# Optimization experiments

Measured on AMD Instinct MI355X. Metric: run time of the kernel, lower is better.

Reference implementation:

```python
import jax, jax.numpy as jnp
import numpy as np

C = 256; NH = 8; HD = C // NH; NL = 4; NP = 4; DFF = 1024
B = 8; NQ = 900
SHAPES = ((100, 100), (50, 50), (25, 25), (13, 13))
LEN = sum(h * w for h, w in SHAPES)


def setup_inputs() -> dict:
    key = jax.random.key(0)
    ks = jax.random.split(key, 16)
    s = 0.02
    d = {}
    d['tgt'] = jax.random.normal(ks[0], (B, NQ, C), jnp.float32)
    d['query_pos'] = jax.random.normal(ks[1], (B, NQ, C), jnp.float32)
    d['reference_points'] = jax.random.uniform(ks[2], (B, NQ, NL, 2), jnp.float32)
    d['src'] = jax.random.normal(ks[3], (B, LEN, C), jnp.float32)
    d['spatial_shapes'] = np.array(SHAPES, dtype=np.int32)
    # self-attn (nn.MultiheadAttention) params, stored [in,out]
    d['sa_in_w'] = jax.random.normal(ks[4], (C, 3 * C), jnp.float32) * s
    d['sa_in_b'] = jnp.zeros((3 * C,), jnp.float32)
    d['sa_out_w'] = jax.random.normal(ks[5], (C, C), jnp.float32) * s
    d['sa_out_b'] = jnp.zeros((C,), jnp.float32)
    d['ln2_g'] = jnp.ones((C,), jnp.float32); d['ln2_b'] = jnp.zeros((C,), jnp.float32)
    # MSDeformAttn params
    d['off_w'] = jax.random.normal(ks[6], (C, NH * NL * NP * 2), jnp.float32) * s
    d['off_b'] = jax.random.normal(ks[7], (NH * NL * NP * 2,), jnp.float32) * 0.5
    d['attw_w'] = jax.random.normal(ks[8], (C, NH * NL * NP), jnp.float32) * s
    d['attw_b'] = jnp.zeros((NH * NL * NP,), jnp.float32)
    d['val_w'] = jax.random.normal(ks[9], (C, C), jnp.float32) * s
    d['val_b'] = jnp.zeros((C,), jnp.float32)
    d['proj_w'] = jax.random.normal(ks[10], (C, C), jnp.float32) * s
    d['proj_b'] = jnp.zeros((C,), jnp.float32)
    d['ln1_g'] = jnp.ones((C,), jnp.float32); d['ln1_b'] = jnp.zeros((C,), jnp.float32)
    # FFN
    d['lin1_w'] = jax.random.normal(ks[11], (C, DFF), jnp.float32) * s
    d['lin1_b'] = jnp.zeros((DFF,), jnp.float32)
    d['lin2_w'] = jax.random.normal(ks[12], (DFF, C), jnp.float32) * s
    d['lin2_b'] = jnp.zeros((C,), jnp.float32)
    d['ln3_g'] = jnp.ones((C,), jnp.float32); d['ln3_b'] = jnp.zeros((C,), jnp.float32)
    return d


def _ln(x, g, b):
    m = jnp.mean(x, -1, keepdims=True)
    v = jnp.mean((x - m) ** 2, -1, keepdims=True)
    return (x - m) * jax.lax.rsqrt(v + 1e-5) * g + b


def _bilinear(v, loc, H, W):
    # v: [B,NH,H*W,HD]; loc: [B,NQ,NH,NP,2] normalized to [0,1]
    # matches F.grid_sample(align_corners=False, padding_mode='zeros')
    b = v.shape[0]; nq = loc.shape[1]
    x = loc[..., 0] * W - 0.5
    y = loc[..., 1] * H - 0.5
    x0 = jnp.floor(x); y0 = jnp.floor(y)
    dx = x - x0; dy = y - y0
    x0i = x0.astype(jnp.int32); y0i = y0.astype(jnp.int32)

    def gat(ix, iy):
        valid = ((ix >= 0) & (ix < W) & (iy >= 0) & (iy < H)).astype(v.dtype)
        idx = jnp.clip(iy, 0, H - 1) * W + jnp.clip(ix, 0, W - 1)  # [B,NQ,NH,NP]
        idx_t = jnp.transpose(idx, (0, 2, 1, 3)).reshape(b, NH, nq * NP)
        g = jnp.take_along_axis(v, idx_t[..., None], axis=2).reshape(b, NH, nq, NP, HD)
        return g * jnp.transpose(valid, (0, 2, 1, 3))[..., None]

    wt = lambda a: jnp.transpose(a, (0, 2, 1, 3))[..., None]
    return (gat(x0i, y0i) * wt((1 - dx) * (1 - dy))
            + gat(x0i + 1, y0i) * wt(dx * (1 - dy))
            + gat(x0i, y0i + 1) * wt((1 - dx) * dy)
            + gat(x0i + 1, y0i + 1) * wt(dx * dy))


def _msda(q, ref, src, shapes, val_w, val_b, off_w, off_b, attw_w, attw_b, proj_w, proj_b):
    b, nq, _ = q.shape
    value = jnp.transpose((src @ val_w + val_b).reshape(b, -1, NH, HD), (0, 2, 1, 3))  # [B,NH,Len,HD]
    off = (q @ off_w + off_b).reshape(b, nq, NH, NL, NP, 2)
    aw = jax.nn.softmax((q @ attw_w + attw_b).reshape(b, nq, NH, NL * NP), -1)
    aw = aw.reshape(b, nq, NH, NL, NP)
    acc = jnp.zeros((b, NH, nq, HD), q.dtype)
    start = 0
    for l, (H_, W_) in enumerate(shapes):
        norm = jnp.array([W_, H_], q.dtype)
        loc = ref[:, :, None, l, None, :] + off[:, :, :, l] / norm  # [B,NQ,NH,NP,2]
        smp = _bilinear(value[:, :, start:start + H_ * W_], loc, H_, W_)  # [B,NH,NQ,NP,HD]
        acc = acc + jnp.sum(smp * jnp.transpose(aw[:, :, :, l], (0, 2, 1, 3))[..., None], axis=3)
        start += H_ * W_
    out = jnp.transpose(acc, (0, 2, 1, 3)).reshape(b, nq, C)
    return out @ proj_w + proj_b


def _self_attn(x, pos, in_w, in_b, out_w, out_b):
    b, nq, _ = x.shape
    qk = x + pos
    q = (qk @ in_w[:, :C] + in_b[:C]).reshape(b, nq, NH, HD)
    k = (qk @ in_w[:, C:2 * C] + in_b[C:2 * C]).reshape(b, nq, NH, HD)
    v = (x @ in_w[:, 2 * C:] + in_b[2 * C:]).reshape(b, nq, NH, HD)
    att = jax.nn.softmax(jnp.einsum('bqhd,bkhd->bhqk', q, k) * (1.0 / float(np.sqrt(HD))), -1)
    o = jnp.einsum('bhqk,bkhd->bqhd', att, v).reshape(b, nq, C)
    return o @ out_w + out_b


def _forward(tgt, query_pos, reference_points, src, shapes,
             sa_in_w, sa_in_b, sa_out_w, sa_out_b, ln2_g, ln2_b,
             off_w, off_b, attw_w, attw_b, val_w, val_b, proj_w, proj_b, ln1_g, ln1_b,
             lin1_w, lin1_b, lin2_w, lin2_b, ln3_g, ln3_b):
    t2 = _self_attn(tgt, query_pos, sa_in_w, sa_in_b, sa_out_w, sa_out_b)
    t = _ln(tgt + t2, ln2_g, ln2_b)
    t2 = _msda(t + query_pos, reference_points, src, shapes,
               val_w, val_b, off_w, off_b, attw_w, attw_b, proj_w, proj_b)
    t = _ln(t + t2, ln1_g, ln1_b)
    h = jax.nn.relu(t @ lin1_w + lin1_b) @ lin2_w + lin2_b
    return _ln(t + h, ln3_g, ln3_b)


def reference(tgt, query_pos, reference_points, src, spatial_shapes,
              sa_in_w, sa_in_b, sa_out_w, sa_out_b, ln2_g, ln2_b,
              off_w, off_b, attw_w, attw_b, val_w, val_b, proj_w, proj_b, ln1_g, ln1_b,
              lin1_w, lin1_b, lin2_w, lin2_b, ln3_g, ln3_b):
    shapes = [(int(h), int(w)) for h, w in np.asarray(spatial_shapes)]
    return _forward(tgt, query_pos, reference_points, src, shapes,
                    sa_in_w, sa_in_b, sa_out_w, sa_out_b, ln2_g, ln2_b,
                    off_w, off_b, attw_w, attw_b, val_w, val_b, proj_w, proj_b, ln1_g, ln1_b,
                    lin1_w, lin1_b, lin2_w, lin2_b, ln3_g, ln3_b)
```

## Files before the change

### kernel.cpp

```cpp
#include <hip/hip_runtime.h>
#include <hip/hip_bf16.h>
#include <type_traits>

#define C_DIM 256
#define NHEAD 8
#define HDIM 32
#define NLVL 4
#define NPT 4
#define DFF_DIM 1024
#define BB 8
#define NQ_DIM 900
#define LEN_DIM 13294
#define ROWS (BB * NQ_DIM)
#define VROWS (BB * LEN_DIM)
#define VT_LD 928

typedef __attribute__((ext_vector_type(8))) short short8v;
typedef __attribute__((ext_vector_type(8))) unsigned short ushort8v;
typedef __attribute__((ext_vector_type(4))) float float4v;
typedef __attribute__((ext_vector_type(4))) unsigned short ushort4v;

__device__ __forceinline__ float bf2f(unsigned short u) {
  union { unsigned int i; float f; } v; v.i = ((unsigned int)u) << 16; return v.f;
}
__device__ __forceinline__ unsigned short f2bf(float f) {
  __hip_bfloat16 h = __float2bfloat16(f);
  return *reinterpret_cast<unsigned short*>(&h);
}

#define WCONV_BLOCKS 2048
__global__ __launch_bounds__(256) void wprep_kernel(
    const float* __restrict__ w0, const float* __restrict__ w1,
    const float* __restrict__ w2, const float* __restrict__ w3,
    const float* __restrict__ w4, const float* __restrict__ w5,
    const float* __restrict__ w6, const float* __restrict__ w7,
    unsigned short* __restrict__ out,
    const float* __restrict__ tgt, const float* __restrict__ qpos,
    unsigned short* __restrict__ tgtbf, unsigned short* __restrict__ x0bf, int n4) {
  int bid = blockIdx.x;
  if (bid < WCONV_BLOCKS) {
    const int Ks[8] = {256, 256, 256, 256, 256, 256, 256, 1024};
    const int Ns[8] = {768, 256, 256, 128, 256, 256, 1024, 256};
    const int Oo[8] = {0, 196608, 262144, 327680, 360448, 425984, 491520, 753664};
    int w = bid >> 8, bx = bid & 255;
    int K = Ks[w], N = Ns[w];
    int ntx = N >> 5, nty = K >> 5;
    if (bx >= ntx * nty) return;
    int tx = bx % ntx, ty = bx / ntx;
    const float* W = w == 0 ? w0 : w == 1 ? w1 : w == 2 ? w2 : w == 3 ? w3
                   : w == 4 ? w4 : w == 5 ? w5 : w == 6 ? w6 : w7;
    __shared__ float tile[32][33];
    int c = threadIdx.x & 31, rg = threadIdx.x >> 5;
#pragma unroll
    for (int j = 0; j < 4; ++j) {
      int k = ty * 32 + rg * 4 + j;
      tile[rg * 4 + j][c] = W[(size_t)k * N + tx * 32 + c];
    }
    __syncthreads();
    unsigned short* o = out + Oo[w];
#pragma unroll
    for (int j = 0; j < 4; ++j) {
      int n = tx * 32 + rg * 4 + j;
      o[(size_t)n * K + ty * 32 + c] = f2bf(tile[c][rg * 4 + j]);
    }
  } else {
    int i = (bid - WCONV_BLOCKS) * 256 + threadIdx.x;
    if (i < n4) {
      float4 x = reinterpret_cast<const float4*>(tgt)[i];
      float4 y = reinterpret_cast<const float4*>(qpos)[i];
      ushort4v u1, u2;
      u1[0] = f2bf(x.x); u1[1] = f2bf(x.y); u1[2] = f2bf(x.z); u1[3] = f2bf(x.w);
      u2[0] = f2bf(x.x + y.x); u2[1] = f2bf(x.y + y.y);
      u2[2] = f2bf(x.z + y.z); u2[3] = f2bf(x.w + y.w);
      *reinterpret_cast<ushort4v*>(tgtbf + (size_t)i * 4) = u1;
      *reinterpret_cast<ushort4v*>(x0bf + (size_t)i * 4) = u2;
    }
  }
}

template <typename TA, typename TO, int RELU>
__device__ __forceinline__ void gemm_body(
    unsigned short* smem,
    const TA* __restrict__ A,
    const unsigned short* __restrict__ Wt,
    const float* __restrict__ bias,
    TO* __restrict__ Cout,
    int M, int N, int K, int lda, int ldc,
    int bx, int by) {
  auto Al = reinterpret_cast<unsigned short(*)[128][40]>(smem);
  auto Wl = reinterpret_cast<unsigned short(*)[128][40]>(smem + 10240);
  const int tid = threadIdx.x;
  const int lane = tid & 63, wid = tid >> 6;
  const int g = lane >> 4, ql = lane & 15;
  const int wr = wid >> 1, wc = wid & 1;
  const int row0 = by * 128, col0 = bx * 128;

  float4v acc[4][4];
#pragma unroll
  for (int i = 0; i < 4; ++i)
#pragma unroll
    for (int j = 0; j < 4; ++j) acc[i][j] = (float4v){0.f, 0.f, 0.f, 0.f};

  float4 areg_f[4];
  ushort8v areg_b[2];
  ushort8v wreg[2];

  auto loadA = [&](int k0) {
    if constexpr (std::is_same<TA, float>::value) {
#pragma unroll
      for (int j = 0; j < 4; ++j) {
        int c = tid + 256 * j;
        int row = c >> 3, f4 = c & 7;
        int gr = min(row0 + row, M - 1);
        areg_f[j] = *reinterpret_cast<const float4*>(A + (size_t)gr * lda + k0 + f4 * 4);
      }
    } else {
#pragma unroll
      for (int j = 0; j < 2; ++j) {
        int c = tid + 256 * j;
        int row = c >> 2, ch = c & 3;
        int gr = min(row0 + row, M - 1);
        areg_b[j] = *reinterpret_cast<const ushort8v*>(
            reinterpret_cast<const unsigned short*>(A) + (size_t)gr * lda + k0 + ch * 8);
      }
    }
  };
  auto loadW = [&](int k0) {
#pragma unroll
    for (int j = 0; j < 2; ++j) {
      int c = tid + 256 * j;
      int row = c >> 2, ch = c & 3;
      wreg[j] = *reinterpret_cast<const ushort8v*>(
          Wt + (size_t)(col0 + row) * K + k0 + ch * 8);
    }
  };
  auto storeA = [&](int buf) {
    if constexpr (std::is_same<TA, float>::value) {
#pragma unroll
      for (int j = 0; j < 4; ++j) {
        int c = tid + 256 * j;
        int row = c >> 3, f4 = c & 7;
        ushort4v u;
        u[0] = f2bf(areg_f[j].x); u[1] = f2bf(areg_f[j].y);
        u[2] = f2bf(areg_f[j].z); u[3] = f2bf(areg_f[j].w);
        *reinterpret_cast<ushort4v*>(&Al[buf][row][f4 * 4]) = u;
      }
    } else {
#pragma unroll
      for (int j = 0; j < 2; ++j) {
        int c = tid + 256 * j;
        int row = c >> 2, ch = c & 3;
        *reinterpret_cast<ushort8v*>(&Al[buf][row][ch * 8]) = areg_b[j];
      }
    }
  };
  auto storeW = [&](int buf) {
#pragma unroll
    for (int j = 0; j < 2; ++j) {
      int c = tid + 256 * j;
      int row = c >> 2, ch = c & 3;
      *reinterpret_cast<ushort8v*>(&Wl[buf][row][ch * 8]) = wreg[j];
    }
  };

  const int nt = K >> 5;
  loadA(0); loadW(0);
  storeA(0); storeW(0);

  for (int t = 0; t < nt; ++t) {
    __syncthreads();
    if (t + 1 < nt) { loadA((t + 1) << 5); loadW((t + 1) << 5); }
    const int cur = t & 1;
    short8v af[4], bfr[4];
#pragma unroll
    for (int mi = 0; mi < 4; ++mi)
      af[mi] = *reinterpret_cast<const short8v*>(&Al[cur][wr * 64 + mi * 16 + ql][8 * g]);
#pragma unroll
    for (int ni = 0; ni < 4; ++ni)
      bfr[ni] = *reinterpret_cast<const short8v*>(&Wl[cur][wc * 64 + ni * 16 + ql][8 * g]);
#pragma unroll
    for (int mi = 0; mi < 4; ++mi)
#pragma unroll
      for (int ni = 0; ni < 4; ++ni)
        acc[mi][ni] = __builtin_amdgcn_mfma_f32_16x16x32_bf16(af[mi], bfr[ni], acc[mi][ni], 0, 0, 0);
    if (t + 1 < nt) { storeA(cur ^ 1); storeW(cur ^ 1); }
  }

  float bv[4];
#pragma unroll
  for (int ni = 0; ni < 4; ++ni) bv[ni] = bias[col0 + wc * 64 + ni * 16 + ql];
#pragma unroll
  for (int mi = 0; mi < 4; ++mi) {
#pragma unroll
    for (int r = 0; r < 4; ++r) {
      int row = row0 + wr * 64 + mi * 16 + 4 * g + r;
      if (row >= M) continue;
#pragma unroll
      for (int ni = 0; ni < 4; ++ni) {
        int col = col0 + wc * 64 + ni * 16 + ql;
        float v = acc[mi][ni][r] + bv[ni];
        if (RELU) v = fmaxf(v, 0.f);
        if constexpr (std::is_same<TO, float>::value) {
          Cout[(size_t)row * ldc + col] = v;
        } else {
          Cout[(size_t)row * ldc + col] = __float2bfloat16(v);
        }
      }
    }
  }
}

template <typename TA, typename TO, int RELU>
__device__ __forceinline__ void gemm_body64(
    unsigned short* smem,
    const TA* __restrict__ A, const TA* __restrict__ A2,
    const unsigned short* __restrict__ Wt,
    const float* __restrict__ bias, const float* __restrict__ bias2,
    TO* __restrict__ Cout, TO* __restrict__ Cout2,
    int M, int N, int K, int lda, int ldc, int ldc2, int colSplit,
    int bx, int by) {
  auto Al = reinterpret_cast<unsigned short(*)[64][40]>(smem);
  auto Wl = reinterpret_cast<unsigned short(*)[64][40]>(smem + 5120);
  const int tid = threadIdx.x;
  const int lane = tid & 63, wid = tid >> 6;
  const int g = lane >> 4, ql = lane & 15;
  const int wr = wid >> 1, wc = wid & 1;
  const int row0 = by * 64, col0 = bx * 64;

  const TA* Ause = (A2 != nullptr && col0 >= colSplit) ? A2 : A;

  float4v acc[2][2];
#pragma unroll
  for (int i = 0; i < 2; ++i)
#pragma unroll
    for (int j = 0; j < 2; ++j) acc[i][j] = (float4v){0.f, 0.f, 0.f, 0.f};

  float4 areg_f[2];
  ushort8v areg_b;
  ushort8v wreg;
  const int a_row = tid >> 2, a_ch = tid & 3;
  const int f_row = tid >> 3, f_f4 = tid & 7;

  auto loadA = [&](int k0) {
    if constexpr (std::is_same<TA, float>::value) {
#pragma unroll
      for (int j = 0; j < 2; ++j) {
        int c = tid + 256 * j;
        int row = c >> 3, f4 = c & 7;
        int gr = min(row0 + row, M - 1);
        areg_f[j] = *reinterpret_cast<const float4*>(Ause + (size_t)gr * lda + k0 + f4 * 4);
      }
    } else {
      int gr = min(row0 + a_row, M - 1);
      areg_b = *reinterpret_cast<const ushort8v*>(
          reinterpret_cast<const unsigned short*>(Ause) + (size_t)gr * lda + k0 + a_ch * 8);
    }
  };
  auto loadW = [&](int k0) {
    wreg = *reinterpret_cast<const ushort8v*>(
        Wt + (size_t)(col0 + a_row) * K + k0 + a_ch * 8);
  };
  auto storeA = [&](int buf) {
    if constexpr (std::is_same<TA, float>::value) {
#pragma unroll
      for (int j = 0; j < 2; ++j) {
        int c = tid + 256 * j;
        int row = c >> 3, f4 = c & 7;
        ushort4v u;
        u[0] = f2bf(areg_f[j].x); u[1] = f2bf(areg_f[j].y);
        u[2] = f2bf(areg_f[j].z); u[3] = f2bf(areg_f[j].w);
        *reinterpret_cast<ushort4v*>(&Al[buf][row][f4 * 4]) = u;
      }
    } else {
      *reinterpret_cast<ushort8v*>(&Al[buf][a_row][a_ch * 8]) = areg_b;
    }
  };
  auto storeW = [&](int buf) {
    *reinterpret_cast<ushort8v*>(&Wl[buf][a_row][a_ch * 8]) = wreg;
  };

  const int nt = K >> 5;
  loadA(0); loadW(0);
  storeA(0); storeW(0);

  for (int t = 0; t < nt; ++t) {
    __syncthreads();
    if (t + 1 < nt) { loadA((t + 1) << 5); loadW((t + 1) << 5); }
    const int cur = t & 1;
    short8v af[2], bfr[2];
#pragma unroll
    for (int mi = 0; mi < 2; ++mi)
      af[mi] = *reinterpret_cast<const short8v*>(&Al[cur][wr * 32 + mi * 16 + ql][8 * g]);
#pragma unroll
    for (int ni = 0; ni < 2; ++ni)
      bfr[ni] = *reinterpret_cast<const short8v*>(&Wl[cur][wc * 32 + ni * 16 + ql][8 * g]);
#pragma unroll
    for (int mi = 0; mi < 2; ++mi)
#pragma unroll
      for (int ni = 0; ni < 2; ++ni)
        acc[mi][ni] = __builtin_amdgcn_mfma_f32_16x16x32_bf16(af[mi], bfr[ni], acc[mi][ni], 0, 0, 0);
    if (t + 1 < nt) { storeA(cur ^ 1); storeW(cur ^ 1); }
  }

  const bool sel2 = (Cout2 != nullptr && col0 >= colSplit);
  const float* bsrc = sel2 ? bias2 : bias;
  TO* outp = sel2 ? Cout2 : Cout;
  const int ldco = sel2 ? ldc2 : ldc;
  const int cbase = sel2 ? (col0 - colSplit) : col0;
  float bv[2];
#pragma unroll
  for (int ni = 0; ni < 2; ++ni) bv[ni] = bsrc[cbase + wc * 32 + ni * 16 + ql];
#pragma unroll
  for (int mi = 0; mi < 2; ++mi) {
#pragma unroll
    for (int r = 0; r < 4; ++r) {
      int row = row0 + wr * 32 + mi * 16 + 4 * g + r;
      if (row >= M) continue;
#pragma unroll
      for (int ni = 0; ni < 2; ++ni) {
        int col = cbase + wc * 32 + ni * 16 + ql;
        float v = acc[mi][ni][r] + bv[ni];
        if (RELU) v = fmaxf(v, 0.f);
        if constexpr (std::is_same<TO, float>::value) {
          outp[(size_t)row * ldco + col] = v;
        } else {
          outp[(size_t)row * ldco + col] = __float2bfloat16(v);
        }
      }
    }
  }
}

template <typename TA, typename TO, int RELU>
__global__ __launch_bounds__(256) void mfma_gemm64_kernel(
    const TA* __restrict__ A, const TA* __restrict__ A2,
    const unsigned short* __restrict__ Wt,
    const float* __restrict__ bias, const float* __restrict__ bias2,
    TO* __restrict__ Cout, TO* __restrict__ Cout2,
    int M, int N, int K, int lda, int ldc, int ldc2, int colSplit) {
  __shared__ unsigned short smem[10240];
  gemm_body64<TA, TO, RELU>(smem, A, A2, Wt, bias, bias2, Cout, Cout2,
                            M, N, K, lda, ldc, ldc2, colSplit,
                            blockIdx.x, blockIdx.y);
}

__device__ __forceinline__ void attn_body(
    unsigned short* smem,
    const unsigned short* __restrict__ qk, const unsigned short* __restrict__ vT,
    unsigned short* __restrict__ out, int qt, int bh) {
  auto P_lds = reinterpret_cast<unsigned short(*)[16][32]>(smem);
  const int tid = threadIdx.x;
  const int lane = tid & 63, wid = tid >> 6;
  const int g = lane >> 4, ql = lane & 15;
  const int b = bh >> 3, h = bh & 7;
  const int q0 = qt * 64 + wid * 16;
  const float scale = 0.17677669529663687f;

  const unsigned short* qk_b = qk + (size_t)b * NQ_DIM * 512;
  const int qrow = min(q0 + ql, NQ_DIM - 1);
  short8v qf = *reinterpret_cast<const short8v*>(
      qk_b + (size_t)qrow * 512 + h * HDIM + 8 * g);
  const unsigned short* kb = qk_b + 256 + h * HDIM + 8 * g;
  const unsigned short* vtb0 = vT + ((size_t)b * 256 + h * HDIM + ql) * VT_LD;
  const unsigned short* vtb1 = vtb0 + 16 * VT_LD;

  float4v o0 = {0.f, 0.f, 0.f, 0.f}, o1 = {0.f, 0.f, 0.f, 0.f};
  float m = -1e30f, lsum = 0.f;

  const int NT = 29;
  for (int kt = 0; kt < NT; ++kt) {
    const int k_base = kt * 32;
    int kr0 = min(k_base + ql, NQ_DIM - 1);
    int kr1 = min(k_base + 16 + ql, NQ_DIM - 1);
    short8v kf0 = *reinterpret_cast<const short8v*>(kb + (size_t)kr0 * 512);
    short8v kf1 = *reinterpret_cast<const short8v*>(kb + (size_t)kr1 * 512);
    float4v z = {0.f, 0.f, 0.f, 0.f};
    float4v s0 = __builtin_amdgcn_mfma_f32_16x16x32_bf16(kf0, qf, z, 0, 0, 0);
    float4v s1 = __builtin_amdgcn_mfma_f32_16x16x32_bf16(kf1, qf, z, 0, 0, 0);

    float s[8];
#pragma unroll
    for (int r = 0; r < 4; ++r) { s[r] = s0[r] * scale; s[4 + r] = s1[r] * scale; }
    if (kt == NT - 1) {
#pragma unroll
      for (int i = 0; i < 8; ++i) {
        int kk = k_base + 16 * (i >> 2) + 4 * g + (i & 3);
        if (kk >= NQ_DIM) s[i] = -1e30f;
      }
    }
    float tm = s[0];
#pragma unroll
    for (int i = 1; i < 8; ++i) tm = fmaxf(tm, s[i]);
    tm = fmaxf(tm, __shfl_xor(tm, 16));
    tm = fmaxf(tm, __shfl_xor(tm, 32));
    float mnew = fmaxf(m, tm);
    float alpha = __expf(m - mnew);
    float p[8];
    float ts = 0.f;
#pragma unroll
    for (int i = 0; i < 8; ++i) { p[i] = __expf(s[i] - mnew); ts += p[i]; }
    ts += __shfl_xor(ts, 16);
    ts += __shfl_xor(ts, 32);
    lsum = lsum * alpha + ts;
    m = mnew;

    ushort4v pp0, pp1;
#pragma unroll
    for (int r = 0; r < 4; ++r) { pp0[r] = f2bf(p[r]); pp1[r] = f2bf(p[4 + r]); }
    *reinterpret_cast<ushort4v*>(&P_lds[wid][ql][4 * g]) = pp0;
    *reinterpret_cast<ushort4v*>(&P_lds[wid][ql][16 + 4 * g]) = pp1;
    asm volatile("s_waitcnt lgkmcnt(0)" ::: "memory");
    __builtin_amdgcn_sched_barrier(0);

    o0 *= alpha;
    o1 *= alpha;

    short8v pf = *reinterpret_cast<const short8v*>(&P_lds[wid][ql][8 * g]);
    short8v vf0 = *reinterpret_cast<const short8v*>(vtb0 + k_base + 8 * g);
    short8v vf1 = *reinterpret_cast<const short8v*>(vtb1 + k_base + 8 * g);
    o0 = __builtin_amdgcn_mfma_f32_16x16x32_bf16(vf0, pf, o0, 0, 0, 0);
    o1 = __builtin_amdgcn_mfma_f32_16x16x32_bf16(vf1, pf, o1, 0, 0, 0);
  }

  float inv = 1.f / lsum;
  if (q0 + ql < NQ_DIM) {
    unsigned short* op = out + ((size_t)(b * NQ_DIM) + q0 + ql) * C_DIM + h * HDIM;
    ushort4v u0, u1;
#pragma unroll
    for (int r = 0; r < 4; ++r) { u0[r] = f2bf(o0[r] * inv); u1[r] = f2bf(o1[r] * inv); }
    *reinterpret_cast<ushort4v*>(op + 4 * g) = u0;
    *reinterpret_cast<ushort4v*>(op + 16 + 4 * g) = u1;
  }
}

#define VAL_BLOCKS (2 * 831)
__global__ __launch_bounds__(256) void value_attn_kernel(
    const float* __restrict__ src, const unsigned short* __restrict__ valT,
    const float* __restrict__ val_b, __hip_bfloat16* __restrict__ value,
    const unsigned short* __restrict__ qkbuf, const unsigned short* __restrict__ vTbuf,
    unsigned short* __restrict__ attnout) {
  __shared__ unsigned short smem[20480];
  int bid = blockIdx.x;
  if (bid < VAL_BLOCKS) {
    gemm_body<float, __hip_bfloat16, 0>(
        smem, src, valT, val_b, value,
        VROWS, 256, 256, 256, 256, bid & 1, bid >> 1);
  } else {
    int a = bid - VAL_BLOCKS;
    attn_body(smem, qkbuf, vTbuf, attnout, a % 15, a / 15);
  }
}

__global__ __launch_bounds__(256) void vtrans_kernel(
    const unsigned short* __restrict__ vbuf, unsigned short* __restrict__ vT) {
  __shared__ unsigned short tile[32][34];
  int b = blockIdx.y;
  int ct = blockIdx.x & 7;
  int rt = blockIdx.x >> 3;
  int rl = threadIdx.x >> 3, c4 = (threadIdx.x & 7) * 4;
  int gr = min(rt * 32 + rl, NQ_DIM - 1);
  ushort4v v = *reinterpret_cast<const ushort4v*>(
      vbuf + ((size_t)(b * NQ_DIM + gr)) * 256 + ct * 32 + c4);
  tile[rl][c4] = v[0]; tile[rl][c4 + 1] = v[1];
  tile[rl][c4 + 2] = v[2]; tile[rl][c4 + 3] = v[3];
  __syncthreads();
  int cl = threadIdx.x >> 3, r4 = (threadIdx.x & 7) * 4;
  ushort4v o;
  o[0] = tile[r4][cl]; o[1] = tile[r4 + 1][cl];
  o[2] = tile[r4 + 2][cl]; o[3] = tile[r4 + 3][cl];
  *reinterpret_cast<ushort4v*>(
      vT + ((size_t)b * 256 + ct * 32 + cl) * VT_LD + rt * 32 + r4) = o;
}

__global__ __launch_bounds__(256) void ln_fused_kernel(const float* __restrict__ x,
                                                       const float* __restrict__ y,
                                                       const float* __restrict__ gg,
                                                       const float* __restrict__ bb,
                                                       float* __restrict__ out,
                                                       unsigned short* __restrict__ out2,
                                                       const float* __restrict__ qadd) {
  int row = blockIdx.x, t = threadIdx.x;
  size_t base = (size_t)row * C_DIM + t;
  float v = x[base] + y[base];
  float s = v, s2 = v * v;
#pragma unroll
  for (int o = 32; o > 0; o >>= 1) {
    s += __shfl_xor(s, o);
    s2 += __shfl_xor(s2, o);
  }
  __shared__ float w1[4], w2[4];
  int wid = t >> 6, lane = t & 63;
  if (lane == 0) { w1[wid] = s; w2[wid] = s2; }
  __syncthreads();
  float S = w1[0] + w1[1] + w1[2] + w1[3];
  float S2 = w2[0] + w2[1] + w2[2] + w2[3];
  float mean = S * (1.f / 256.f);
  float var = S2 * (1.f / 256.f) - mean * mean;
  float rstd = rsqrtf(var + 1e-5f);
  float r = (v - mean) * rstd * gg[t] + bb[t];
  out[base] = r;
  if (out2) {
    float r2 = qadd ? (r + qadd[base]) : r;
    out2[base] = f2bf(r2);
  }
}

__global__ __launch_bounds__(256) void softmax16_kernel(float* __restrict__ aw, int total) {
  int t = blockIdx.x * 256 + threadIdx.x;
  if (t >= total) return;
  float* p = aw + (size_t)t * 16;
  float vals[16];
  float m = -1e30f;
#pragma unroll
  for (int i = 0; i < 16; ++i) { vals[i] = p[i]; m = fmaxf(m, vals[i]); }
  float s = 0.f;
#pragma unroll
  for (int i = 0; i < 16; ++i) { vals[i] = __expf(vals[i] - m); s += vals[i]; }
  float inv = 1.f / s;
#pragma unroll
  for (int i = 0; i < 16; ++i) p[i] = vals[i] * inv;
}

__global__ __launch_bounds__(256) void msda_sample_kernel(
    const unsigned short* __restrict__ value,
    const float* __restrict__ off,
    const float* __restrict__ aw,
    const float* __restrict__ refp,
    const int* __restrict__ shapes,
    unsigned short* __restrict__ out) {
  int g = blockIdx.x * 64 + (threadIdx.x >> 2);
  int d8 = threadIdx.x & 3;
  int h = g & 7;
  int row = g >> 3;
  int b = row / NQ_DIM;
  float acc[8] = {};
  int start = 0;
  const float* offr = off + (size_t)row * 256 + h * 32;
  const float* awr  = aw + (size_t)row * 128 + h * 16;
  const float* rpr  = refp + (size_t)row * NLVL * 2;
#pragma unroll
  for (int l = 0; l < NLVL; ++l) {
    int Hl = shapes[2 * l], Wl = shapes[2 * l + 1];
    float fx = rpr[2 * l + 0] * (float)Wl - 0.5f;
    float fy = rpr[2 * l + 1] * (float)Hl - 0.5f;
    const unsigned short* vbase =
        value + ((size_t)(b * LEN_DIM + start)) * C_DIM + h * HDIM + d8 * 8;
#pragma unroll
    for (int p = 0; p < NPT; ++p) {
      float x = fx + offr[l * 8 + p * 2];
      float y = fy + offr[l * 8 + p * 2 + 1];
      float a = awr[l * 4 + p];
      float x0f = floorf(x), y0f = floorf(y);
      float dx = x - x0f, dy = y - y0f;
      int x0 = (int)x0f, y0 = (int)y0f;
      int x1 = x0 + 1, y1 = y0 + 1;
      float wx1 = dx, wx0 = 1.f - dx;
      float wy1 = dy * a, wy0 = (1.f - dy) * a;
      bool vx0 = ((unsigned)x0 < (unsigned)Wl);
      bool vx1 = ((unsigned)x1 < (unsigned)Wl);
      bool vy0 = ((unsigned)y0 < (unsigned)Hl);
      bool vy1 = ((unsigned)y1 < (unsigned)Hl);
      float w00 = (vx0 && vy0) ? wx0 * wy0 : 0.f;
      float w10 = (vx1 && vy0) ? wx1 * wy0 : 0.f;
      float w01 = (vx0 && vy1) ? wx0 * wy1 : 0.f;
      float w11 = (vx1 && vy1) ? wx1 * wy1 : 0.f;
      int x0c = min(max(x0, 0), Wl - 1), x1c = min(max(x1, 0), Wl - 1);
      int y0c = min(max(y0, 0), Hl - 1), y1c = min(max(y1, 0), Hl - 1);
      int r0 = y0c * Wl, r1 = y1c * Wl;
      ushort8v g00 = *reinterpret_cast<const ushort8v*>(vbase + ((r0 + x0c) << 8));
      ushort8v g10 = *reinterpret_cast<const ushort8v*>(vbase + ((r0 + x1c) << 8));
      ushort8v g01 = *reinterpret_cast<const ushort8v*>(vbase + ((r1 + x0c) << 8));
      ushort8v g11 = *reinterpret_cast<const ushort8v*>(vbase + ((r1 + x1c) << 8));
#pragma unroll
      for (int j = 0; j < 8; ++j)
        acc[j] += w00 * bf2f(g00[j]) + w10 * bf2f(g10[j]) +
                  w01 * bf2f(g01[j]) + w11 * bf2f(g11[j]);
    }
    start += Hl * Wl;
  }
  ushort8v o;
#pragma unroll
  for (int j = 0; j < 8; ++j) o[j] = f2bf(acc[j]);
  *reinterpret_cast<ushort8v*>(out + (size_t)row * C_DIM + h * HDIM + d8 * 8) = o;
}

extern "C" void kernel_launch(void* const* d_in, const int* in_sizes, int n_in,
                              void* d_out, int out_size, void* d_ws, size_t ws_size,
                              hipStream_t stream) {
  const float* tgt      = (const float*)d_in[0];
  const float* qpos     = (const float*)d_in[1];
  const float* refp     = (const float*)d_in[2];
  const float* src      = (const float*)d_in[3];
  const int*   shapes   = (const int*)d_in[4];
  const float* sa_in_w  = (const float*)d_in[5];
  const float* sa_in_b  = (const float*)d_in[6];
  const float* sa_out_w = (const float*)d_in[7];
  const float* sa_out_b = (const float*)d_in[8];
  const float* ln2_g    = (const float*)d_in[9];
  const float* ln2_b    = (const float*)d_in[10];
  const float* off_w    = (const float*)d_in[11];
  const float* off_b    = (const float*)d_in[12];
  const float* attw_w   = (const float*)d_in[13];
  const float* attw_b   = (const float*)d_in[14];
  const float* val_w    = (const float*)d_in[15];
  const float* val_b    = (const float*)d_in[16];
  const float* proj_w   = (const float*)d_in[17];
  const float* proj_b   = (const float*)d_in[18];
  const float* ln1_g    = (const float*)d_in[19];
  const float* ln1_b    = (const float*)d_in[20];
  const float* lin1_w   = (const float*)d_in[21];
  const float* lin1_b   = (const float*)d_in[22];
  const float* lin2_w   = (const float*)d_in[23];
  const float* lin2_b   = (const float*)d_in[24];
  const float* ln3_g    = (const float*)d_in[25];
  const float* ln3_b    = (const float*)d_in[26];

  char* ws = (char*)d_ws;
  size_t off_b_ws = 0;
  auto alloc = [&](size_t bytes) {
    char* p = ws + off_b_ws;
    off_b_ws += (bytes + 255) & ~(size_t)255;
    return p;
  };
  unsigned short* wT     = (unsigned short*)alloc((size_t)1015808 * 2);
  unsigned short* value  = (unsigned short*)alloc((size_t)VROWS * C_DIM * 2);
  unsigned short* qkbuf  = (unsigned short*)alloc((size_t)ROWS * 512 * 2);
  unsigned short* vbuf   = (unsigned short*)alloc((size_t)ROWS * 256 * 2);
  unsigned short* vTbuf  = (unsigned short*)alloc((size_t)BB * 256 * VT_LD * 2);
  unsigned short* tgtbf  = (unsigned short*)alloc((size_t)ROWS * C_DIM * 2);
  unsigned short* X0bf   = (unsigned short*)alloc((size_t)ROWS * C_DIM * 2);
  unsigned short* attnbf = (unsigned short*)alloc((size_t)ROWS * C_DIM * 2);
  unsigned short* X3bf   = (unsigned short*)alloc((size_t)ROWS * C_DIM * 2);
  unsigned short* sampbf = (unsigned short*)alloc((size_t)ROWS * C_DIM * 2);
  unsigned short* X6bf   = (unsigned short*)alloc((size_t)ROWS * C_DIM * 2);
  unsigned short* hidbf  = (unsigned short*)alloc((size_t)ROWS * DFF_DIM * 2);
  float* X1 = (float*)alloc((size_t)ROWS * C_DIM * 4);
  float* X2 = (float*)alloc((size_t)ROWS * C_DIM * 4);
  float* X4 = (float*)alloc((size_t)ROWS * C_DIM * 4);
  float* X5 = (float*)alloc((size_t)ROWS * 128 * 4);
  float* X6 = (float*)alloc((size_t)ROWS * C_DIM * 4);
  if (off_b_ws > ws_size) return;

  unsigned short* sa_inT = wT + 0;
  unsigned short* sa_outT = wT + 196608;
  unsigned short* offT   = wT + 262144;
  unsigned short* valT   = wT + 360448;
  unsigned short* projT  = wT + 425984;
  unsigned short* lin1T  = wT + 491520;
  unsigned short* lin2T  = wT + 753664;

  dim3 blk(256);
  const int MB64 = (ROWS + 63) / 64;
  int n4 = ROWS * C_DIM / 4;
  int prepBlocks = (n4 + 255) / 256;

  wprep_kernel<<<WCONV_BLOCKS + prepBlocks, blk, 0, stream>>>(
      sa_in_w, sa_out_w, off_w, attw_w, val_w, proj_w, lin1_w, lin2_w, wT,
      tgt, qpos, tgtbf, X0bf, n4);

  mfma_gemm64_kernel<unsigned short, __hip_bfloat16, 0><<<dim3(12, MB64), blk, 0, stream>>>(
      X0bf, tgtbf, sa_inT, sa_in_b, sa_in_b + 512,
      (__hip_bfloat16*)qkbuf, (__hip_bfloat16*)vbuf, ROWS, 768, 256, 256, 512, 256, 512);

  vtrans_kernel<<<dim3(8 * 29, BB), blk, 0, stream>>>(vbuf, vTbuf);

  value_attn_kernel<<<VAL_BLOCKS + 15 * 64, blk, 0, stream>>>(
      src, valT, val_b, (__hip_bfloat16*)value, qkbuf, vTbuf, attnbf);

  mfma_gemm64_kernel<unsigned short, float, 0><<<dim3(4, MB64), blk, 0, stream>>>(
      attnbf, nullptr, sa_outT, sa_out_b, nullptr,
      X1, nullptr, ROWS, 256, 256, 256, 256, 0, 1 << 30);
  ln_fused_kernel<<<ROWS, blk, 0, stream>>>(tgt, X1, ln2_g, ln2_b, X2, X3bf, qpos);

  mfma_gemm64_kernel<unsigned short, float, 0><<<dim3(6, MB64), blk, 0, stream>>>(
      X3bf, nullptr, offT, off_b, attw_b,
      X4, X5, ROWS, 384, 256, 256, 256, 128, 256);
  softmax16_kernel<<<(ROWS * NHEAD + 255) / 256, blk, 0, stream>>>(X5, ROWS * NHEAD);
  msda_sample_kernel<<<ROWS * NHEAD / 64, blk, 0, stream>>>(
      value, X4, X5, refp, shapes, sampbf);
  mfma_gemm64_kernel<unsigned short, float, 0><<<dim3(4, MB64), blk, 0, stream>>>(
      sampbf, nullptr, projT, proj_b, nullptr,
      X1, nullptr, ROWS, 256, 256, 256, 256, 0, 1 << 30);
  ln_fused_kernel<<<ROWS, blk, 0, stream>>>(X2, X1, ln1_g, ln1_b, X6, X6bf, nullptr);

  mfma_gemm64_kernel<unsigned short, __hip_bfloat16, 1><<<dim3(16, MB64), blk, 0, stream>>>(
      X6bf, nullptr, lin1T, lin1_b, nullptr,
      (__hip_bfloat16*)hidbf, nullptr, ROWS, 1024, 256, 256, 1024, 0, 1 << 30);
  mfma_gemm64_kernel<unsigned short, float, 0><<<dim3(4, MB64), blk, 0, stream>>>(
      hidbf, nullptr, lin2T, lin2_b, nullptr,
      X1, nullptr, ROWS, 256, 1024, 1024, 256, 0, 1 << 30);
  ln_fused_kernel<<<ROWS, blk, 0, stream>>>(X6, X1, ln3_g, ln3_b, (float*)d_out, nullptr, nullptr);
}
```

Baseline: 231.6 us.

## Co-schedule QKV projection with value GEMM; split self-attention into own kernel

The QKV projection now runs as 128x128 tiles in the same launch as the large value-projection GEMM, instead of as a separate 64x64-tile GEMM launch. Self-attention moves out of the value kernel into its own MFMA kernel that runs after the V transpose. The aim is to overlap the small QKV GEMM with the large value GEMM and to use bigger tiles for QKV, at the cost of no longer overlapping attention with the value GEMM. The 128-tile GEMM body gains A/output splitting so it can write Q/K and V to separate buffers.

```diff
diff --git a/kernel.cpp b/kernel.cpp
--- a/kernel.cpp
+++ b/kernel.cpp
@@ -81,11 +81,11 @@
 template <typename TA, typename TO, int RELU>
 __device__ __forceinline__ void gemm_body(
     unsigned short* smem,
-    const TA* __restrict__ A,
+    const TA* __restrict__ A, const TA* __restrict__ A2,
     const unsigned short* __restrict__ Wt,
-    const float* __restrict__ bias,
-    TO* __restrict__ Cout,
-    int M, int N, int K, int lda, int ldc,
+    const float* __restrict__ bias, const float* __restrict__ bias2,
+    TO* __restrict__ Cout, TO* __restrict__ Cout2,
+    int M, int N, int K, int lda, int ldc, int ldc2, int colSplit,
     int bx, int by) {
   auto Al = reinterpret_cast<unsigned short(*)[128][40]>(smem);
   auto Wl = reinterpret_cast<unsigned short(*)[128][40]>(smem + 10240);
@@ -95,6 +95,8 @@
   const int wr = wid >> 1, wc = wid & 1;
   const int row0 = by * 128, col0 = bx * 128;
 
+  const TA* Ause = (A2 != nullptr && col0 >= colSplit) ? A2 : A;
+
   float4v acc[4][4];
 #pragma unroll
   for (int i = 0; i < 4; ++i)
@@ -112,7 +114,7 @@
         int c = tid + 256 * j;
         int row = c >> 3, f4 = c & 7;
         int gr = min(row0 + row, M - 1);
-        areg_f[j] = *reinterpret_cast<const float4*>(A + (size_t)gr * lda + k0 + f4 * 4);
+        areg_f[j] = *reinterpret_cast<const float4*>(Ause + (size_t)gr * lda + k0 + f4 * 4);
       }
     } else {
 #pragma unroll
@@ -121,7 +123,7 @@
         int row = c >> 2, ch = c & 3;
         int gr = min(row0 + row, M - 1);
         areg_b[j] = *reinterpret_cast<const ushort8v*>(
-            reinterpret_cast<const unsigned short*>(A) + (size_t)gr * lda + k0 + ch * 8);
+            reinterpret_cast<const unsigned short*>(Ause) + (size_t)gr * lda + k0 + ch * 8);
       }
     }
   };
@@ -186,9 +188,14 @@
     if (t + 1 < nt) { storeA(cur ^ 1); storeW(cur ^ 1); }
   }
 
+  const bool sel2 = (Cout2 != nullptr && col0 >= colSplit);
+  const float* bsrc = sel2 ? bias2 : bias;
+  TO* outp = sel2 ? Cout2 : Cout;
+  const int ldco = sel2 ? ldc2 : ldc;
+  const int cbase = sel2 ? (col0 - colSplit) : col0;
   float bv[4];
 #pragma unroll
-  for (int ni = 0; ni < 4; ++ni) bv[ni] = bias[col0 + wc * 64 + ni * 16 + ql];
+  for (int ni = 0; ni < 4; ++ni) bv[ni] = bsrc[cbase + wc * 64 + ni * 16 + ql];
 #pragma unroll
   for (int mi = 0; mi < 4; ++mi) {
 #pragma unroll
@@ -197,13 +204,13 @@
       if (row >= M) continue;
 #pragma unroll
       for (int ni = 0; ni < 4; ++ni) {
-        int col = col0 + wc * 64 + ni * 16 + ql;
+        int col = cbase + wc * 64 + ni * 16 + ql;
         float v = acc[mi][ni][r] + bv[ni];
         if (RELU) v = fmaxf(v, 0.f);
         if constexpr (std::is_same<TO, float>::value) {
-          Cout[(size_t)row * ldc + col] = v;
+          outp[(size_t)row * ldco + col] = v;
         } else {
-          Cout[(size_t)row * ldc + col] = __float2bfloat16(v);
+          outp[(size_t)row * ldco + col] = __float2bfloat16(v);
         }
       }
     }
@@ -239,7 +246,6 @@
   ushort8v areg_b;
   ushort8v wreg;
   const int a_row = tid >> 2, a_ch = tid & 3;
-  const int f_row = tid >> 3, f_f4 = tid & 7;
 
   auto loadA = [&](int k0) {
     if constexpr (std::is_same<TA, float>::value) {
@@ -344,110 +350,24 @@
                             blockIdx.x, blockIdx.y);
 }
 
-__device__ __forceinline__ void attn_body(
-    unsigned short* smem,
-    const unsigned short* __restrict__ qk, const unsigned short* __restrict__ vT,
-    unsigned short* __restrict__ out, int qt, int bh) {
-  auto P_lds = reinterpret_cast<unsigned short(*)[16][32]>(smem);
-  const int tid = threadIdx.x;
-  const int lane = tid & 63, wid = tid >> 6;
-  const int g = lane >> 4, ql = lane & 15;
-  const int b = bh >> 3, h = bh & 7;
-  const int q0 = qt * 64 + wid * 16;
-  const float scale = 0.17677669529663687f;
-
-  const unsigned short* qk_b = qk + (size_t)b * NQ_DIM * 512;
-  const int qrow = min(q0 + ql, NQ_DIM - 1);
-  short8v qf = *reinterpret_cast<const short8v*>(
-      qk_b + (size_t)qrow * 512 + h * HDIM + 8 * g);
-  const unsigned short* kb = qk_b + 256 + h * HDIM + 8 * g;
-  const unsigned short* vtb0 = vT + ((size_t)b * 256 + h * HDIM + ql) * VT_LD;
-  const unsigned short* vtb1 = vtb0 + 16 * VT_LD;
-
-  float4v o0 = {0.f, 0.f, 0.f, 0.f}, o1 = {0.f, 0.f, 0.f, 0.f};
-  float m = -1e30f, lsum = 0.f;
-
-  const int NT = 29;
-  for (int kt = 0; kt < NT; ++kt) {
-    const int k_base = kt * 32;
-    int kr0 = min(k_base + ql, NQ_DIM - 1);
-    int kr1 = min(k_base + 16 + ql, NQ_DIM - 1);
-    short8v kf0 = *reinterpret_cast<const short8v*>(kb + (size_t)kr0 * 512);
-    short8v kf1 = *reinterpret_cast<const short8v*>(kb + (size_t)kr1 * 512);
-    float4v z = {0.f, 0.f, 0.f, 0.f};
-    float4v s0 = __builtin_amdgcn_mfma_f32_16x16x32_bf16(kf0, qf, z, 0, 0, 0);
-    float4v s1 = __builtin_amdgcn_mfma_f32_16x16x32_bf16(kf1, qf, z, 0, 0, 0);
-
-    float s[8];
-#pragma unroll
-    for (int r = 0; r < 4; ++r) { s[r] = s0[r] * scale; s[4 + r] = s1[r] * scale; }
-    if (kt == NT - 1) {
-#pragma unroll
-      for (int i = 0; i < 8; ++i) {
-        int kk = k_base + 16 * (i >> 2) + 4 * g + (i & 3);
-        if (kk >= NQ_DIM) s[i] = -1e30f;
-      }
-    }
-    float tm = s[0];
-#pragma unroll
-    for (int i = 1; i < 8; ++i) tm = fmaxf(tm, s[i]);
-    tm = fmaxf(tm, __shfl_xor(tm, 16));
-    tm = fmaxf(tm, __shfl_xor(tm, 32));
-    float mnew = fmaxf(m, tm);
-    float alpha = __expf(m - mnew);
-    float p[8];
-    float ts = 0.f;
-#pragma unroll
-    for (int i = 0; i < 8; ++i) { p[i] = __expf(s[i] - mnew); ts += p[i]; }
-    ts += __shfl_xor(ts, 16);
-    ts += __shfl_xor(ts, 32);
-    lsum = lsum * alpha + ts;
-    m = mnew;
-
-    ushort4v pp0, pp1;
-#pragma unroll
-    for (int r = 0; r < 4; ++r) { pp0[r] = f2bf(p[r]); pp1[r] = f2bf(p[4 + r]); }
-    *reinterpret_cast<ushort4v*>(&P_lds[wid][ql][4 * g]) = pp0;
-    *reinterpret_cast<ushort4v*>(&P_lds[wid][ql][16 + 4 * g]) = pp1;
-    asm volatile("s_waitcnt lgkmcnt(0)" ::: "memory");
-    __builtin_amdgcn_sched_barrier(0);
-
-    o0 *= alpha;
-    o1 *= alpha;
-
-    short8v pf = *reinterpret_cast<const short8v*>(&P_lds[wid][ql][8 * g]);
-    short8v vf0 = *reinterpret_cast<const short8v*>(vtb0 + k_base + 8 * g);
-    short8v vf1 = *reinterpret_cast<const short8v*>(vtb1 + k_base + 8 * g);
-    o0 = __builtin_amdgcn_mfma_f32_16x16x32_bf16(vf0, pf, o0, 0, 0, 0);
-    o1 = __builtin_amdgcn_mfma_f32_16x16x32_bf16(vf1, pf, o1, 0, 0, 0);
-  }
-
-  float inv = 1.f / lsum;
-  if (q0 + ql < NQ_DIM) {
-    unsigned short* op = out + ((size_t)(b * NQ_DIM) + q0 + ql) * C_DIM + h * HDIM;
-    ushort4v u0, u1;
-#pragma unroll
-    for (int r = 0; r < 4; ++r) { u0[r] = f2bf(o0[r] * inv); u1[r] = f2bf(o1[r] * inv); }
-    *reinterpret_cast<ushort4v*>(op + 4 * g) = u0;
-    *reinterpret_cast<ushort4v*>(op + 16 + 4 * g) = u1;
-  }
-}
-
-#define VAL_BLOCKS (2 * 831)
-__global__ __launch_bounds__(256) void value_attn_kernel(
+#define QKV_BLOCKS (6 * 57)
+__global__ __launch_bounds__(256) void qkv_value_kernel(
+    const unsigned short* __restrict__ x0bf, const unsigned short* __restrict__ tgtbf,
+    const unsigned short* __restrict__ sa_inT, const float* __restrict__ sa_in_b,
+    __hip_bfloat16* __restrict__ qkbuf, __hip_bfloat16* __restrict__ vbuf,
     const float* __restrict__ src, const unsigned short* __restrict__ valT,
-    const float* __restrict__ val_b, __hip_bfloat16* __restrict__ value,
-    const unsigned short* __restrict__ qkbuf, const unsigned short* __restrict__ vTbuf,
-    unsigned short* __restrict__ attnout) {
+    const float* __restrict__ val_b, __hip_bfloat16* __restrict__ value) {
   __shared__ unsigned short smem[20480];
   int bid = blockIdx.x;
-  if (bid < VAL_BLOCKS) {
+  if (bid < QKV_BLOCKS) {
+    gemm_body<unsigned short, __hip_bfloat16, 0>(
+        smem, x0bf, tgtbf, sa_inT, sa_in_b, sa_in_b + 512, qkbuf, vbuf,
+        ROWS, 768, 256, 256, 512, 256, 512, bid % 6, bid / 6);
+  } else {
+    int t = bid - QKV_BLOCKS;
     gemm_body<float, __hip_bfloat16, 0>(
-        smem, src, valT, val_b, value,
-        VROWS, 256, 256, 256, 256, bid & 1, bid >> 1);
-  } else {
-    int a = bid - VAL_BLOCKS;
-    attn_body(smem, qkbuf, vTbuf, attnout, a % 15, a / 15);
+        smem, src, nullptr, valT, val_b, nullptr, value, nullptr,
+        VROWS, 256, 256, 256, 256, 0, 1 << 30, t & 1, t >> 1);
   }
 }
 
@@ -502,6 +422,95 @@
   if (out2) {
     float r2 = qadd ? (r + qadd[base]) : r;
     out2[base] = f2bf(r2);
+  }
+}
+
+__global__ __launch_bounds__(256) void self_attn_mfma_kernel(
+    const unsigned short* __restrict__ qk, const unsigned short* __restrict__ vT,
+    unsigned short* __restrict__ out) {
+  __shared__ unsigned short P_lds[4][16][32];
+  const int tid = threadIdx.x;
+  const int lane = tid & 63, wid = tid >> 6;
+  const int g = lane >> 4, ql = lane & 15;
+  const int bh = blockIdx.y;
+  const int b = bh >> 3, h = bh & 7;
+  const int q0 = blockIdx.x * 64 + wid * 16;
+  const float scale = 0.17677669529663687f;
+
+  const unsigned short* qk_b = qk + (size_t)b * NQ_DIM * 512;
+  const int qrow = min(q0 + ql, NQ_DIM - 1);
+  short8v qf = *reinterpret_cast<const short8v*>(
+      qk_b + (size_t)qrow * 512 + h * HDIM + 8 * g);
+  const unsigned short* kb = qk_b + 256 + h * HDIM + 8 * g;
+  const unsigned short* vtb0 = vT + ((size_t)b * 256 + h * HDIM + ql) * VT_LD;
+  const unsigned short* vtb1 = vtb0 + 16 * VT_LD;
+
+  float4v o0 = {0.f, 0.f, 0.f, 0.f}, o1 = {0.f, 0.f, 0.f, 0.f};
+  float m = -1e30f, lsum = 0.f;
+
+  const int NT = 29;
+  for (int kt = 0; kt < NT; ++kt) {
+    const int k_base = kt * 32;
+    int kr0 = min(k_base + ql, NQ_DIM - 1);
+    int kr1 = min(k_base + 16 + ql, NQ_DIM - 1);
+    short8v kf0 = *reinterpret_cast<const short8v*>(kb + (size_t)kr0 * 512);
+    short8v kf1 = *reinterpret_cast<const short8v*>(kb + (size_t)kr1 * 512);
+    float4v z = {0.f, 0.f, 0.f, 0.f};
+    float4v s0 = __builtin_amdgcn_mfma_f32_16x16x32_bf16(kf0, qf, z, 0, 0, 0);
+    float4v s1 = __builtin_amdgcn_mfma_f32_16x16x32_bf16(kf1, qf, z, 0, 0, 0);
+
+    float s[8];
+#pragma unroll
+    for (int r = 0; r < 4; ++r) { s[r] = s0[r] * scale; s[4 + r] = s1[r] * scale; }
+    if (kt == NT - 1) {
+#pragma unroll
+      for (int i = 0; i < 8; ++i) {
+        int kk = k_base + 16 * (i >> 2) + 4 * g + (i & 3);
+        if (kk >= NQ_DIM) s[i] = -1e30f;
+      }
+    }
+    float tm = s[0];
+#pragma unroll
+    for (int i = 1; i < 8; ++i) tm = fmaxf(tm, s[i]);
+    tm = fmaxf(tm, __shfl_xor(tm, 16));
+    tm = fmaxf(tm, __shfl_xor(tm, 32));
+    float mnew = fmaxf(m, tm);
+    float alpha = __expf(m - mnew);
+    float p[8];
+    float ts = 0.f;
+#pragma unroll
+    for (int i = 0; i < 8; ++i) { p[i] = __expf(s[i] - mnew); ts += p[i]; }
+    ts += __shfl_xor(ts, 16);
+    ts += __shfl_xor(ts, 32);
+    lsum = lsum * alpha + ts;
+    m = mnew;
+
+    ushort4v pp0, pp1;
+#pragma unroll
+    for (int r = 0; r < 4; ++r) { pp0[r] = f2bf(p[r]); pp1[r] = f2bf(p[4 + r]); }
+    *reinterpret_cast<ushort4v*>(&P_lds[wid][ql][4 * g]) = pp0;
+    *reinterpret_cast<ushort4v*>(&P_lds[wid][ql][16 + 4 * g]) = pp1;
+    asm volatile("s_waitcnt lgkmcnt(0)" ::: "memory");
+    __builtin_amdgcn_sched_barrier(0);
+
+    o0 *= alpha;
+    o1 *= alpha;
+
+    short8v pf = *reinterpret_cast<const short8v*>(&P_lds[wid][ql][8 * g]);
+    short8v vf0 = *reinterpret_cast<const short8v*>(vtb0 + k_base + 8 * g);
+    short8v vf1 = *reinterpret_cast<const short8v*>(vtb1 + k_base + 8 * g);
+    o0 = __builtin_amdgcn_mfma_f32_16x16x32_bf16(vf0, pf, o0, 0, 0, 0);
+    o1 = __builtin_amdgcn_mfma_f32_16x16x32_bf16(vf1, pf, o1, 0, 0, 0);
+  }
+
+  float inv = 1.f / lsum;
+  if (q0 + ql < NQ_DIM) {
+    unsigned short* op = out + ((size_t)(b * NQ_DIM) + q0 + ql) * C_DIM + h * HDIM;
+    ushort4v u0, u1;
+#pragma unroll
+    for (int r = 0; r < 4; ++r) { u0[r] = f2bf(o0[r] * inv); u1[r] = f2bf(o1[r] * inv); }
+    *reinterpret_cast<ushort4v*>(op + 4 * g) = u0;
+    *reinterpret_cast<ushort4v*>(op + 16 + 4 * g) = u1;
   }
 }
 
@@ -650,6 +659,7 @@
   unsigned short* lin2T  = wT + 753664;
 
   dim3 blk(256);
+  const int MBV = (VROWS + 127) / 128;
   const int MB64 = (ROWS + 63) / 64;
   int n4 = ROWS * C_DIM / 4;
   int prepBlocks = (n4 + 255) / 256;
@@ -658,14 +668,13 @@
       sa_in_w, sa_out_w, off_w, attw_w, val_w, proj_w, lin1_w, lin2_w, wT,
       tgt, qpos, tgtbf, X0bf, n4);
 
-  mfma_gemm64_kernel<unsigned short, __hip_bfloat16, 0><<<dim3(12, MB64), blk, 0, stream>>>(
-      X0bf, tgtbf, sa_inT, sa_in_b, sa_in_b + 512,
-      (__hip_bfloat16*)qkbuf, (__hip_bfloat16*)vbuf, ROWS, 768, 256, 256, 512, 256, 512);
+  qkv_value_kernel<<<QKV_BLOCKS + 2 * MBV, blk, 0, stream>>>(
+      X0bf, tgtbf, sa_inT, sa_in_b, (__hip_bfloat16*)qkbuf, (__hip_bfloat16*)vbuf,
+      src, valT, val_b, (__hip_bfloat16*)value);
 
   vtrans_kernel<<<dim3(8 * 29, BB), blk, 0, stream>>>(vbuf, vTbuf);
 
-  value_attn_kernel<<<VAL_BLOCKS + 15 * 64, blk, 0, stream>>>(
-      src, valT, val_b, (__hip_bfloat16*)value, qkbuf, vTbuf, attnbf);
+  self_attn_mfma_kernel<<<dim3(15, 64), blk, 0, stream>>>(qkbuf, vTbuf, attnbf);
 
   mfma_gemm64_kernel<unsigned short, float, 0><<<dim3(4, MB64), blk, 0, stream>>>(
       attnbf, nullptr, sa_outT, sa_out_b, nullptr,
```

Result: faster. 221.5 us (-4.4%).
